# Performance work log

Measured on AMD Instinct MI355X. Metric: run time of the kernel, lower is better.

## Reference

```python
import jax, jax.numpy as jnp
import numpy as np

N_WIN = 8  # matches init kwarg n_win

def setup_inputs() -> dict:
    key = jax.random.key(0)
    k1, k2, k3 = jax.random.split(key, 3)
    c = 64
    x = jax.random.normal(k1, (1, c, 256, 256), dtype=jnp.float32)
    W = jax.random.normal(k2, (3 * c, c), dtype=jnp.float32) * 0.05
    bias = jax.random.normal(k3, (3 * c,), dtype=jnp.float32) * 0.05
    return {"x": x, "W": W, "bias": bias}

def reference(x, W, bias):
    b, c, h, w = x.shape
    n_h = n_w = N_WIN
    hs, ws = h // n_h, w // n_w
    nw = n_h * n_w
    # unfold into non-overlapping windows: [1, nw, hs*ws, c]
    xw = x.reshape(b, c, n_h, hs, n_w, ws)
    xw = xw.transpose(0, 2, 4, 3, 5, 1).reshape(1, nw, hs * ws, c)
    # shared QKV linear
    qkv = xw @ W.T + bias
    q, k, v = qkv[..., :c], qkv[..., c:2 * c], qkv[..., 2 * c:3 * c]
    # region-level routing via mean-pooled tokens
    q_r = q.mean(axis=2)  # [1, nw, c]
    k_r = k.mean(axis=2)
    a_r = jax.nn.relu(jnp.einsum('bic,bjc->bij', q_r, k_r))  # [1, nw, nw]
    # mix windows: a_r @ flattened(k/q) == window-mixing einsum
    k_m = jnp.einsum('bij,bjtc->bitc', a_r, k)
    q_m = jnp.einsum('bij,bjtc->bitc', a_r, q)
    # relu-gated windowed attention
    attn = jax.nn.relu(jnp.einsum('bitc,bisc->bits', q_m, k_m))  # [1, nw, T, T]
    o = jnp.einsum('bits,bisc->bitc', attn, v)  # [1, nw, T, c]
    # fold back to image
    o = o.reshape(b, n_h, n_w, hs, ws, c).transpose(0, 5, 1, 3, 2, 4).reshape(b, c, h, w)
    return o
```

## Files before the change

### kernel.cpp

```cpp
#include <hip/hip_runtime.h>

typedef _Float16 half_t;
typedef __attribute__((ext_vector_type(8))) _Float16 half8;
typedef __attribute__((ext_vector_type(4))) _Float16 half4;
typedef __attribute__((ext_vector_type(4))) float floatx4;
typedef __attribute__((ext_vector_type(16))) float floatx16;

#define MFMA16(A, B, C) __builtin_amdgcn_mfma_f32_16x16x32_f16((A), (B), (C), 0, 0, 0)
#define MFMA32(A, B, C) __builtin_amdgcn_mfma_f32_32x32x16_f16((A), (B), (C), 0, 0, 0)

__global__ __launch_bounds__(256) void k_qkv(
    const float* __restrict__ x, const float* __restrict__ W,
    const float* __restrict__ bias, half_t* __restrict__ q,
    half_t* __restrict__ k, half_t* __restrict__ vT,
    float* __restrict__ qp, float* __restrict__ kp) {
  __shared__ __align__(16) half_t Xs[128][72];
  __shared__ __align__(16) half_t Ws[192][72];
  __shared__ float qs_l[64], ks_l[64];
  const int w = blockIdx.y;
  const int tx = blockIdx.x;
  const int t0 = tx * 128;
  const int ih = w >> 3, iw = w & 7;
  const int xbase = ih * 8192 + iw * 32;
  const int tid = threadIdx.x;

  for (int i = tid; i < 8192; i += 256) {
    const int c = i >> 7, tt = i & 127;
    const int t = t0 + tt;
    Xs[tt][c] = (half_t)x[c * 65536 + xbase + (t >> 5) * 256 + (t & 31)];
  }
  for (int i = tid; i < 3072; i += 256) {
    const int o = i >> 4, c4 = (i & 15) * 4;
    const floatx4 v = *(const floatx4*)&W[o * 64 + c4];
    half4 hv;
    #pragma unroll
    for (int p = 0; p < 4; p++) hv[p] = (half_t)v[p];
    *(half4*)&Ws[o][c4] = hv;
  }
  if (tid < 64) { qs_l[tid] = 0.f; ks_l[tid] = 0.f; }
  __syncthreads();

  const int wave = tid >> 6, lane = tid & 63;
  const int lrow = lane & 15, lq = lane >> 4;
  const int rbase = (wave >> 1) * 64;
  const int cbase = (wave & 1) * 96;

  floatx4 acc[4][6];
  const floatx4 z = {0.f, 0.f, 0.f, 0.f};
  #pragma unroll
  for (int mt = 0; mt < 4; mt++)
    #pragma unroll
    for (int nt = 0; nt < 6; nt++) acc[mt][nt] = z;

  #pragma unroll
  for (int kf = 0; kf < 2; kf++) {
    const int koff = kf * 32 + lq * 8;
    half8 a[4], b[6];
    #pragma unroll
    for (int mt = 0; mt < 4; mt++)
      a[mt] = *(const half8*)&Xs[rbase + mt * 16 + lrow][koff];
    #pragma unroll
    for (int nt = 0; nt < 6; nt++)
      b[nt] = *(const half8*)&Ws[cbase + nt * 16 + lrow][koff];
    #pragma unroll
    for (int mt = 0; mt < 4; mt++)
      #pragma unroll
      for (int nt = 0; nt < 6; nt++)
        acc[mt][nt] = MFMA16(a[mt], b[nt], acc[mt][nt]);
  }

  #pragma unroll
  for (int nt = 0; nt < 6; nt++) {
    const int o = cbase + nt * 16 + lrow;
    const float bs = bias[o];
    if (o < 64) {
      float s = 0.f;
      #pragma unroll
      for (int mt = 0; mt < 4; mt++) {
        const int tr = t0 + rbase + mt * 16 + lq * 4;
        #pragma unroll
        for (int r = 0; r < 4; r++) {
          const float v = acc[mt][nt][r] + bs;
          q[w * 65536 + (tr + r) * 64 + o] = (half_t)v;
          s += v;
        }
      }
      atomicAdd(&qs_l[o], s);
    } else if (o < 128) {
      const int oc = o - 64;
      float s = 0.f;
      #pragma unroll
      for (int mt = 0; mt < 4; mt++) {
        const int tr = t0 + rbase + mt * 16 + lq * 4;
        #pragma unroll
        for (int r = 0; r < 4; r++) {
          const float v = acc[mt][nt][r] + bs;
          k[w * 65536 + (tr + r) * 64 + oc] = (half_t)v;
          s += v;
        }
      }
      atomicAdd(&ks_l[oc], s);
    } else {
      const int oc = o - 128;
      #pragma unroll
      for (int mt = 0; mt < 4; mt++) {
        const int tr = t0 + rbase + mt * 16 + lq * 4;
        half4 pk;
        #pragma unroll
        for (int r = 0; r < 4; r++) pk[r] = (half_t)(acc[mt][nt][r] + bs);
        *(half4*)&vT[w * 65536 + oc * 1024 + tr] = pk;
      }
    }
  }
  __syncthreads();
  if (tid < 64) {
    qp[(w * 8 + tx) * 64 + tid] = qs_l[tid];
    kp[(w * 8 + tx) * 64 + tid] = ks_l[tid];
  }
}

__global__ __launch_bounds__(256) void k_ar(const float* __restrict__ qp,
                                            const float* __restrict__ kp,
                                            half_t* __restrict__ arH) {
  __shared__ float qs[64][65];
  __shared__ float ks[64][65];
  const int tid = threadIdx.x;
  for (int e = tid; e < 4096; e += 256) {
    const int i = e >> 6, c = e & 63;
    float sq = 0.f, sk = 0.f;
    #pragma unroll
    for (int t = 0; t < 8; t++) {
      sq += qp[i * 512 + t * 64 + c];
      sk += kp[i * 512 + t * 64 + c];
    }
    qs[i][c] = sq;
    ks[i][c] = sk;
  }
  __syncthreads();
  const float scale = 1.f / (1024.f * 1024.f);
  const int e = blockIdx.x * 256 + tid;
  const int i = e >> 6, j = e & 63;
  float s = 0.f;
  #pragma unroll
  for (int c = 0; c < 64; c++) s += qs[i][c] * ks[j][c];
  s *= scale;
  arH[e] = (half_t)(s > 0.f ? s : 0.f);
}

__global__ __launch_bounds__(256) void k_mix(const half_t* __restrict__ q,
                                             const half_t* __restrict__ k,
                                             const half_t* __restrict__ arH,
                                             half_t* __restrict__ qm,
                                             half_t* __restrict__ km) {
  const half_t* __restrict__ src = blockIdx.y ? k : q;
  half_t* __restrict__ dst = blockIdx.y ? km : qm;
  const int tid = threadIdx.x;
  const int wave = tid >> 6, lane = tid & 63;
  const int ln31 = lane & 31;
  const int hk8 = (lane >> 5) * 8;

  half8 aA[2][4];
  #pragma unroll
  for (int mt = 0; mt < 2; mt++)
    #pragma unroll
    for (int kk = 0; kk < 4; kk++)
      aA[mt][kk] = *(const half8*)&arH[(mt * 32 + ln31) * 64 + kk * 16 + hk8];

  #pragma unroll
  for (int t32 = 0; t32 < 2; t32++) {
    const int pos = blockIdx.x * 256 + wave * 64 + t32 * 32 + ln31;
    half8 bB[4];
    #pragma unroll
    for (int kk = 0; kk < 4; kk++)
      #pragma unroll
      for (int jj = 0; jj < 8; jj++)
        bB[kk][jj] = src[(kk * 16 + hk8 + jj) * 65536 + pos];

    floatx16 c0, c1;
    #pragma unroll
    for (int r = 0; r < 16; r++) { c0[r] = 0.f; c1[r] = 0.f; }
    #pragma unroll
    for (int kk = 0; kk < 4; kk++) {
      c0 = MFMA32(aA[0][kk], bB[kk], c0);
      c1 = MFMA32(aA[1][kk], bB[kk], c1);
    }
    const int h4 = (lane >> 5) * 4;
    #pragma unroll
    for (int r = 0; r < 16; r++) {
      const int row = (r & 3) + h4 + 8 * (r >> 2);
      dst[row * 65536 + pos] = (half_t)c0[r];
      dst[(32 + row) * 65536 + pos] = (half_t)c1[r];
    }
  }
}

__global__ __launch_bounds__(256, 2) void k_attn(const half_t* __restrict__ qm,
                                                 const half_t* __restrict__ km,
                                                 const half_t* __restrict__ vT,
                                                 float* __restrict__ out) {
  __shared__ __align__(16) half_t Vs[64][136];
  __shared__ __align__(16) half_t St[128][138];
  const int w = blockIdx.y;
  const int t0 = blockIdx.x * 128;
  const int tid = threadIdx.x;
  const int wave = tid >> 6, lane = tid & 63;
  const int ln31 = lane & 31;
  const int hk8 = (lane >> 5) * 8, hk4 = (lane >> 5) * 4;
  const int w32 = wave * 32;
  const int wbase = w * 65536;

  half8 bQ[4][4];
  #pragma unroll
  for (int tt = 0; tt < 4; tt++)
    #pragma unroll
    for (int kk = 0; kk < 4; kk++)
      bQ[tt][kk] = *(const half8*)&qm[wbase + (t0 + tt * 32 + ln31) * 64 + kk * 16 + hk8];

  floatx16 oacc[2];
  #pragma unroll
  for (int ct = 0; ct < 2; ct++)
    #pragma unroll
    for (int r = 0; r < 16; r++) oacc[ct][r] = 0.f;

  for (int sc = 0; sc < 8; sc++) {
    const int s0 = sc * 128;
    __syncthreads();
    for (int idx = tid; idx < 1024; idx += 256) {
      const int c = idx >> 4, so = (idx & 15) * 8;
      *(half8*)&Vs[c][so] = *(const half8*)&vT[wbase + c * 1024 + s0 + so];
    }
    half8 aK[4];
    #pragma unroll
    for (int kk = 0; kk < 4; kk++)
      aK[kk] = *(const half8*)&km[wbase + (s0 + w32 + ln31) * 64 + kk * 16 + hk8];
    __syncthreads();

    floatx16 sacc[4];
    #pragma unroll
    for (int tt = 0; tt < 4; tt++)
      #pragma unroll
      for (int r = 0; r < 16; r++) sacc[tt][r] = 0.f;
    #pragma unroll
    for (int kk = 0; kk < 4; kk++)
      #pragma unroll
      for (int tt = 0; tt < 4; tt++)
        sacc[tt] = MFMA32(aK[kk], bQ[tt][kk], sacc[tt]);

    #pragma unroll
    for (int tt = 0; tt < 4; tt++) {
      const int t = tt * 32 + ln31;
      #pragma unroll
      for (int g = 0; g < 4; g++) {
        const int s = w32 + g * 8 + hk4;
        half4 pk;
        #pragma unroll
        for (int p = 0; p < 4; p++) {
          const float v = sacc[tt][g * 4 + p];
          pk[p] = (half_t)(v > 0.f ? v : 0.f);
        }
        *(half4*)&St[t][s] = pk;
      }
    }
    __syncthreads();

    #pragma unroll
    for (int kk = 0; kk < 8; kk++) {
      const half8 bS = *(const half8*)&St[w32 + ln31][kk * 16 + hk8];
      #pragma unroll
      for (int ct = 0; ct < 2; ct++) {
        const half8 aV = *(const half8*)&Vs[ct * 32 + ln31][kk * 16 + hk8];
        oacc[ct] = MFMA32(aV, bS, oacc[ct]);
      }
    }
  }

  const int ih = w >> 3, iw = w & 7;
  const int obase = ih * 8192 + iw * 32;
  const int tb = ((t0 + w32) >> 5) * 256 + ln31;
  const int h4 = (lane >> 5) * 4;
  #pragma unroll
  for (int ct = 0; ct < 2; ct++) {
    #pragma unroll
    for (int r = 0; r < 16; r++) {
      const int c = ct * 32 + (r & 3) + h4 + 8 * (r >> 2);
      out[c * 65536 + obase + tb] = oacc[ct][r];
    }
  }
}

extern "C" void kernel_launch(void* const* d_in, const int* in_sizes, int n_in,
                              void* d_out, int out_size, void* d_ws, size_t ws_size,
                              hipStream_t stream) {
  const float* x = (const float*)d_in[0];
  const float* W = (const float*)d_in[1];
  const float* bias = (const float*)d_in[2];
  float* out = (float*)d_out;

  half_t* q = (half_t*)d_ws;
  half_t* k = q + 4194304;
  half_t* vT = k + 4194304;
  half_t* qm = vT + 4194304;
  half_t* km = qm + 4194304;
  float* qp = (float*)(km + 4194304);
  float* kp = qp + 32768;
  half_t* arH = (half_t*)(kp + 32768);

  k_qkv<<<dim3(8, 64), 256, 0, stream>>>(x, W, bias, q, k, vT, qp, kp);
  k_ar<<<16, 256, 0, stream>>>(qp, kp, arH);
  k_mix<<<dim3(256, 2), 256, 0, stream>>>(q, k, arH, qm, km);
  k_attn<<<dim3(8, 64), 256, 0, stream>>>(qm, km, vT, out);
}
```

Before: 129.4 us.

## Restructure QKV projection with 32x32 MFMA and coalesced staging; read V directly in attention

The QKV kernel now loads x with per-thread column gathers packed into half8 stores. It computes Q/K as W·X^T and V as X·W^T using 32x32 MFMA tiles. Q/K results are staged through a reused LDS buffer so they can be written out with coalesced half8 stores, and the mean-pool partial sums are taken from the staged tile. The attention kernel drops its LDS V tile and one barrier, reading V fragments straight from global memory (cached). This trades LDS traffic and syncs for more global or cache loads, and it adds an occupancy hint on the QKV kernel.

```diff
diff --git a/kernel.cpp b/kernel.cpp
--- a/kernel.cpp
+++ b/kernel.cpp
@@ -3,31 +3,42 @@
 typedef _Float16 half_t;
 typedef __attribute__((ext_vector_type(8))) _Float16 half8;
 typedef __attribute__((ext_vector_type(4))) _Float16 half4;
+typedef __attribute__((ext_vector_type(2))) _Float16 half2_t;
 typedef __attribute__((ext_vector_type(4))) float floatx4;
 typedef __attribute__((ext_vector_type(16))) float floatx16;
 
-#define MFMA16(A, B, C) __builtin_amdgcn_mfma_f32_16x16x32_f16((A), (B), (C), 0, 0, 0)
 #define MFMA32(A, B, C) __builtin_amdgcn_mfma_f32_32x32x16_f16((A), (B), (C), 0, 0, 0)
 
-__global__ __launch_bounds__(256) void k_qkv(
+__global__ __launch_bounds__(256, 3) void k_qkv(
     const float* __restrict__ x, const float* __restrict__ W,
     const float* __restrict__ bias, half_t* __restrict__ q,
     half_t* __restrict__ k, half_t* __restrict__ vT,
     float* __restrict__ qp, float* __restrict__ kp) {
-  __shared__ __align__(16) half_t Xs[128][72];
-  __shared__ __align__(16) half_t Ws[192][72];
+  __shared__ __align__(16) char smem[46080];
+  half_t (*Xs)[72] = (half_t (*)[72])smem;
+  half_t (*Ws)[72] = (half_t (*)[72])(smem + 18432);
+  half_t (*E1)[136] = (half_t (*)[136])smem;
   __shared__ float qs_l[64], ks_l[64];
-  const int w = blockIdx.y;
-  const int tx = blockIdx.x;
+
+  const int w = blockIdx.y, tx = blockIdx.x;
   const int t0 = tx * 128;
   const int ih = w >> 3, iw = w & 7;
   const int xbase = ih * 8192 + iw * 32;
   const int tid = threadIdx.x;
 
-  for (int i = tid; i < 8192; i += 256) {
-    const int c = i >> 7, tt = i & 127;
-    const int t = t0 + tt;
-    Xs[tt][c] = (half_t)x[c * 65536 + xbase + (t >> 5) * 256 + (t & 31)];
+  if (tid < 64) { qs_l[tid] = 0.f; ks_l[tid] = 0.f; }
+
+  {
+    const int t = tid & 127, cg = tid >> 7;
+    const int tg = t0 + t;
+    const int xoff = xbase + (tg >> 5) * 256 + (tg & 31);
+    half8 h8[4];
+    #pragma unroll
+    for (int m = 0; m < 32; m++)
+      h8[m >> 3][m & 7] = (half_t)x[(cg * 32 + m) * 65536 + xoff];
+    #pragma unroll
+    for (int g = 0; g < 4; g++)
+      *(half8*)&Xs[t][cg * 32 + g * 8] = h8[g];
   }
   for (int i = tid; i < 3072; i += 256) {
     const int o = i >> 4, c4 = (i & 15) * 4;
@@ -37,80 +48,96 @@
     for (int p = 0; p < 4; p++) hv[p] = (half_t)v[p];
     *(half4*)&Ws[o][c4] = hv;
   }
-  if (tid < 64) { qs_l[tid] = 0.f; ks_l[tid] = 0.f; }
   __syncthreads();
 
   const int wave = tid >> 6, lane = tid & 63;
-  const int lrow = lane & 15, lq = lane >> 4;
-  const int rbase = (wave >> 1) * 64;
-  const int cbase = (wave & 1) * 96;
-
-  floatx4 acc[4][6];
-  const floatx4 z = {0.f, 0.f, 0.f, 0.f};
-  #pragma unroll
-  for (int mt = 0; mt < 4; mt++)
-    #pragma unroll
-    for (int nt = 0; nt < 6; nt++) acc[mt][nt] = z;
-
-  #pragma unroll
-  for (int kf = 0; kf < 2; kf++) {
-    const int koff = kf * 32 + lq * 8;
-    half8 a[4], b[6];
-    #pragma unroll
-    for (int mt = 0; mt < 4; mt++)
-      a[mt] = *(const half8*)&Xs[rbase + mt * 16 + lrow][koff];
-    #pragma unroll
-    for (int nt = 0; nt < 6; nt++)
-      b[nt] = *(const half8*)&Ws[cbase + nt * 16 + lrow][koff];
-    #pragma unroll
-    for (int mt = 0; mt < 4; mt++)
-      #pragma unroll
-      for (int nt = 0; nt < 6; nt++)
-        acc[mt][nt] = MFMA16(a[mt], b[nt], acc[mt][nt]);
-  }
-
-  #pragma unroll
-  for (int nt = 0; nt < 6; nt++) {
-    const int o = cbase + nt * 16 + lrow;
-    const float bs = bias[o];
-    if (o < 64) {
-      float s = 0.f;
-      #pragma unroll
-      for (int mt = 0; mt < 4; mt++) {
-        const int tr = t0 + rbase + mt * 16 + lq * 4;
-        #pragma unroll
-        for (int r = 0; r < 4; r++) {
-          const float v = acc[mt][nt][r] + bs;
-          q[w * 65536 + (tr + r) * 64 + o] = (half_t)v;
-          s += v;
-        }
-      }
-      atomicAdd(&qs_l[o], s);
-    } else if (o < 128) {
-      const int oc = o - 64;
-      float s = 0.f;
-      #pragma unroll
-      for (int mt = 0; mt < 4; mt++) {
-        const int tr = t0 + rbase + mt * 16 + lq * 4;
-        #pragma unroll
-        for (int r = 0; r < 4; r++) {
-          const float v = acc[mt][nt][r] + bs;
-          k[w * 65536 + (tr + r) * 64 + oc] = (half_t)v;
-          s += v;
-        }
-      }
-      atomicAdd(&ks_l[oc], s);
-    } else {
-      const int oc = o - 128;
-      #pragma unroll
-      for (int mt = 0; mt < 4; mt++) {
-        const int tr = t0 + rbase + mt * 16 + lq * 4;
+  const int ln31 = lane & 31;
+  const int hk8 = (lane >> 5) * 8, hk4 = (lane >> 5) * 4;
+  const int w32 = wave * 32;
+
+  floatx16 d1[4], dv[2];
+  #pragma unroll
+  for (int tt = 0; tt < 4; tt++)
+    #pragma unroll
+    for (int r = 0; r < 16; r++) d1[tt][r] = 0.f;
+  #pragma unroll
+  for (int ot = 0; ot < 2; ot++)
+    #pragma unroll
+    for (int r = 0; r < 16; r++) dv[ot][r] = 0.f;
+
+  #pragma unroll
+  for (int kk = 0; kk < 4; kk++) {
+    const int ko = kk * 16 + hk8;
+    const half8 aW = *(const half8*)&Ws[w32 + ln31][ko];
+    half8 bX[4];
+    #pragma unroll
+    for (int tt = 0; tt < 4; tt++)
+      bX[tt] = *(const half8*)&Xs[tt * 32 + ln31][ko];
+    const half8 bV0 = *(const half8*)&Ws[128 + ln31][ko];
+    const half8 bV1 = *(const half8*)&Ws[160 + ln31][ko];
+    #pragma unroll
+    for (int tt = 0; tt < 4; tt++) d1[tt] = MFMA32(aW, bX[tt], d1[tt]);
+    dv[0] = MFMA32(bX[wave], bV0, dv[0]);
+    dv[1] = MFMA32(bX[wave], bV1, dv[1]);
+  }
+
+  {
+    const int wbase = w * 65536;
+    #pragma unroll
+    for (int ot = 0; ot < 2; ot++) {
+      const int o = ot * 32 + ln31;
+      const float bv = bias[128 + o];
+      #pragma unroll
+      for (int g = 0; g < 4; g++) {
+        const int tl = w32 + g * 8 + hk4;
         half4 pk;
         #pragma unroll
-        for (int r = 0; r < 4; r++) pk[r] = (half_t)(acc[mt][nt][r] + bs);
-        *(half4*)&vT[w * 65536 + oc * 1024 + tr] = pk;
+        for (int p = 0; p < 4; p++) pk[p] = (half_t)(dv[ot][g * 4 + p] + bv);
+        *(half4*)&vT[wbase + o * 1024 + t0 + tl] = pk;
       }
     }
+  }
+
+  __syncthreads();
+
+  {
+    floatx4 b4[4];
+    #pragma unroll
+    for (int g = 0; g < 4; g++)
+      b4[g] = *(const floatx4*)&bias[w32 + g * 8 + hk4];
+    #pragma unroll
+    for (int tt = 0; tt < 4; tt++) {
+      const int t = tt * 32 + ln31;
+      #pragma unroll
+      for (int g = 0; g < 4; g++) {
+        half4 pk;
+        #pragma unroll
+        for (int p = 0; p < 4; p++)
+          pk[p] = (half_t)(d1[tt][g * 4 + p] + b4[g][p]);
+        *(half4*)&E1[t][w32 + g * 8 + hk4] = pk;
+      }
+    }
+  }
+  __syncthreads();
+
+  {
+    const int colc = tid & 15, tgrp = tid >> 4;
+    const int o8 = (colc & 7) * 8;
+    half_t* __restrict__ base = (colc < 8) ? q : k;
+    float sums[8];
+    #pragma unroll
+    for (int p = 0; p < 8; p++) sums[p] = 0.f;
+    #pragma unroll
+    for (int j = 0; j < 8; j++) {
+      const int t = tgrp * 8 + j;
+      const half8 v8 = *(const half8*)&E1[t][colc * 8];
+      *(half8*)&base[w * 65536 + (t0 + t) * 64 + o8] = v8;
+      #pragma unroll
+      for (int p = 0; p < 8; p++) sums[p] += (float)v8[p];
+    }
+    float* sl = (colc < 8) ? qs_l : ks_l;
+    #pragma unroll
+    for (int p = 0; p < 8; p++) atomicAdd(&sl[o8 + p], sums[p]);
   }
   __syncthreads();
   if (tid < 64) {
@@ -198,8 +225,7 @@
                                                  const half_t* __restrict__ km,
                                                  const half_t* __restrict__ vT,
                                                  float* __restrict__ out) {
-  __shared__ __align__(16) half_t Vs[64][136];
-  __shared__ __align__(16) half_t St[128][138];
+  __shared__ __align__(16) half_t St[128][136];
   const int w = blockIdx.y;
   const int t0 = blockIdx.x * 128;
   const int tid = threadIdx.x;
@@ -224,16 +250,10 @@
 
   for (int sc = 0; sc < 8; sc++) {
     const int s0 = sc * 128;
-    __syncthreads();
-    for (int idx = tid; idx < 1024; idx += 256) {
-      const int c = idx >> 4, so = (idx & 15) * 8;
-      *(half8*)&Vs[c][so] = *(const half8*)&vT[wbase + c * 1024 + s0 + so];
-    }
     half8 aK[4];
     #pragma unroll
     for (int kk = 0; kk < 4; kk++)
       aK[kk] = *(const half8*)&km[wbase + (s0 + w32 + ln31) * 64 + kk * 16 + hk8];
-    __syncthreads();
 
     floatx16 sacc[4];
     #pragma unroll
@@ -246,6 +266,7 @@
       for (int tt = 0; tt < 4; tt++)
         sacc[tt] = MFMA32(aK[kk], bQ[tt][kk], sacc[tt]);
 
+    __syncthreads();
     #pragma unroll
     for (int tt = 0; tt < 4; tt++) {
       const int t = tt * 32 + ln31;
@@ -268,7 +289,7 @@
       const half8 bS = *(const half8*)&St[w32 + ln31][kk * 16 + hk8];
       #pragma unroll
       for (int ct = 0; ct < 2; ct++) {
-        const half8 aV = *(const half8*)&Vs[ct * 32 + ln31][kk * 16 + hk8];
+        const half8 aV = *(const half8*)&vT[wbase + (ct * 32 + ln31) * 1024 + s0 + kk * 16 + hk8];
         oacc[ct] = MFMA32(aV, bS, oacc[ct]);
       }
     }
```

Result: slower. 154.9 us (+19.7%).
